# Kernel tuning notes

Measured on AMD Instinct MI355X. Metric: run time of the kernel, lower is better.

## Reference

```python
import jax, jax.numpy as jnp
import numpy as np

NUM_HEADS = 16
HEAD_DIM = 128
NUM_KV_HEADS = 8
NUM_KV_GROUPS = 2
HIDDEN = 2048
SCALE = 0.5  # hardcoded in the original SDPA call


def _fixed_sincos_pos(E, H):
    # matches ReusedProjReconstructor._fixed_sincos_pos (H even here)
    half = H // 2
    freq = jnp.exp(-jnp.log(jnp.float32(10000.0)) * jnp.arange(half, dtype=jnp.float32) / half)
    pos = jnp.arange(E, dtype=jnp.float32)[:, None]
    ang = pos * freq[None, :]
    return jnp.concatenate([jnp.sin(ang), jnp.cos(ang)], axis=1)  # [E, H]


def setup_inputs() -> dict:
    key = jax.random.key(0)
    ks = jax.random.split(key, 8)
    B, M, H = 4, 2048, HIDDEN
    kv_dim = NUM_KV_HEADS * HEAD_DIM
    s = 0.02
    return {
        "mem_act": jax.random.normal(ks[0], (B, M, H), jnp.float32),
        "Wq": jax.random.normal(ks[1], (H, H), jnp.float32) * s,
        "bq": jax.random.normal(ks[2], (H,), jnp.float32) * s,
        "Wk": jax.random.normal(ks[3], (kv_dim, H), jnp.float32) * s,
        "bk": jax.random.normal(ks[4], (kv_dim,), jnp.float32) * s,
        "Wv": jax.random.normal(ks[5], (kv_dim, H), jnp.float32) * s,
        "bv": jax.random.normal(ks[6], (kv_dim,), jnp.float32) * s,
        "Wo": jax.random.normal(ks[7], (H, H), jnp.float32) * s,
        "E": 2048,
    }


def reference(mem_act, Wq, bq, Wk, bk, Wv, bv, Wo, E):
    B, M, H = mem_act.shape
    # positional query hidden, shared across batch (q_ln is Identity)
    q_hidden = _fixed_sincos_pos(E, H).astype(mem_act.dtype)  # [E, H]
    q = (q_hidden @ Wq.T + bq).reshape(E, NUM_HEADS, HEAD_DIM)          # [E, nh, hd]
    k = (mem_act @ Wk.T + bk).reshape(B, M, NUM_KV_HEADS, HEAD_DIM)     # [B, M, nkv, hd]
    v = (mem_act @ Wv.T + bv).reshape(B, M, NUM_KV_HEADS, HEAD_DIM)
    # GQA: repeat kv heads (repeat_interleave over head dim)
    k = jnp.repeat(k, NUM_KV_GROUPS, axis=2)  # [B, M, nh, hd]
    v = jnp.repeat(v, NUM_KV_GROUPS, axis=2)
    # non-causal SDPA with scale=0.5, query broadcast over batch
    scores = jnp.einsum("ehd,bmhd->bhem", q, k) * SCALE  # [B, nh, E, M]
    attn = jax.nn.softmax(scores, axis=-1)
    out = jnp.einsum("bhem,bmhd->behd", attn, v).reshape(B, E, H)
    pred = out @ Wo.T  # o_proj (no bias, Qwen2 style)
    return pred
```

## Files before the change

### kernel.cpp

```cpp
#include <hip/hip_runtime.h>
#include <hip/hip_bf16.h>

typedef __attribute__((ext_vector_type(8))) short short8;
typedef __attribute__((ext_vector_type(4))) float f32x4;
typedef __attribute__((ext_vector_type(16))) float f32x16;
typedef unsigned short ushort_t;

__device__ __forceinline__ unsigned short f2bf(float x) {
    unsigned int u = __builtin_bit_cast(unsigned int, x);
    unsigned int r = (u + 0x7fffu + ((u >> 16) & 1u)) >> 16;
    return (unsigned short)r;
}

__device__ __forceinline__ void gload_lds16(const ushort_t* g, ushort_t* l) {
    __builtin_amdgcn_global_load_lds(
        (const __attribute__((address_space(1))) void*)g,
        (__attribute__((address_space(3))) void*)l, 16, 0, 0);
}

#define MFMA16(A, B, C) __builtin_amdgcn_mfma_f32_16x16x32_bf16((A), (B), (C), 0, 0, 0)
#define MFMA32(A, B, C) __builtin_amdgcn_mfma_f32_32x32x16_bf16((A), (B), (C), 0, 0, 0)

__global__ __launch_bounds__(256) void prep_all(const float* __restrict__ im,
                                                const float* __restrict__ iq,
                                                const float* __restrict__ ik,
                                                const float* __restrict__ iv,
                                                const float* __restrict__ io,
                                                ushort_t* __restrict__ om,
                                                ushort_t* __restrict__ oq,
                                                ushort_t* __restrict__ ok,
                                                ushort_t* __restrict__ ov,
                                                ushort_t* __restrict__ oo,
                                                ushort_t* __restrict__ qh) {
    const int bid = blockIdx.x;
    if (bid < 14336) {
        long i = ((long)bid * 256 + threadIdx.x) << 3;
        const float* s;
        ushort_t* d;
        if (i < 16777216)      { s = im + i;              d = om + i; }
        else if (i < 20971520) { s = iq + (i - 16777216); d = oq + (i - 16777216); }
        else if (i < 23068672) { s = ik + (i - 20971520); d = ok + (i - 20971520); }
        else if (i < 25165824) { s = iv + (i - 23068672); d = ov + (i - 23068672); }
        else                   { s = io + (i - 25165824); d = oo + (i - 25165824); }
        const float4* p = (const float4*)s;
        float4 a = p[0], b = p[1];
        short8 o;
        o[0] = (short)f2bf(a.x); o[1] = (short)f2bf(a.y);
        o[2] = (short)f2bf(a.z); o[3] = (short)f2bf(a.w);
        o[4] = (short)f2bf(b.x); o[5] = (short)f2bf(b.y);
        o[6] = (short)f2bf(b.z); o[7] = (short)f2bf(b.w);
        *(short8*)d = o;
    } else {
        const int t8 = (bid - 14336) * 256 + threadIdx.x;
        const int e = t8 >> 7;
        const int i0 = (t8 & 127) << 3;
        short8 sv8, cv8;
#pragma unroll
        for (int j = 0; j < 8; ++j) {
            const int i = i0 + j;
            float freq = __expf(-9.2103403719761836f * (float)i * (1.0f / 1024.0f));
            float ang = (float)e * freq;
            float rev = ang * 0.15915494309189535f;
            rev -= floorf(rev);
            float sv, cv;
            asm("v_sin_f32 %0, %1" : "=v"(sv) : "v"(rev));
            asm("v_cos_f32 %0, %1" : "=v"(cv) : "v"(rev));
            sv8[j] = (short)f2bf(sv);
            cv8[j] = (short)f2bf(cv);
        }
        *(short8*)(qh + (size_t)e * 2048 + i0)        = sv8;
        *(short8*)(qh + (size_t)e * 2048 + 1024 + i0) = cv8;
    }
}

__global__ __launch_bounds__(256, 2) void gemm_q(const ushort_t* __restrict__ A,
                                                 const ushort_t* __restrict__ Bw,
                                                 const float* __restrict__ bias,
                                                 ushort_t* __restrict__ Cout,
                                                 int M, int N, int K) {
    __shared__ ushort_t As[4][128 * 32];
    __shared__ ushort_t Bs[4][128 * 32];
    const int tid = threadIdx.x, lane = tid & 63;
    const int wid = tid >> 6;
    const int q5 = lane & 31, hi = lane >> 5;
    const int wm = wid >> 1, wn = wid & 1;
    const int nbn = N >> 7;
    const int nwg = gridDim.x;
    const int swz = (blockIdx.x & 7) * (nwg >> 3) + (blockIdx.x >> 3);
    const int bm = swz / nbn, bn = swz % nbn;
    const int row0 = bm << 7, col0 = bn << 7;
    const int NT = K >> 5;

    f32x16 acc[2][2];
#pragma unroll
    for (int mi = 0; mi < 2; ++mi)
#pragma unroll
        for (int nj = 0; nj < 2; ++nj)
#pragma unroll
            for (int rr = 0; rr < 16; ++rr) acc[mi][nj][rr] = 0.f;

    auto STAGE_HALF = [&](int buf, int kt, int i) {
        const int k0 = kt << 5;
        const int fb = (i * 256 + tid) << 4;
        const int rp = fb >> 7;
        const int bo = ((fb >> 4) & 7) ^ (rp & 7);
        const int row = rp * 2 + (bo >> 2);
        const int kc = (bo & 3) << 3;
        gload_lds16(A  + (size_t)(row0 + row) * K + k0 + kc, &As[buf][0] + (fb >> 1));
        gload_lds16(Bw + (size_t)(col0 + row) * K + k0 + kc, &Bs[buf][0] + (fb >> 1));
    };

    STAGE_HALF(0, 0, 0); STAGE_HALF(0, 0, 1);
    STAGE_HALF(1, 1, 0); STAGE_HALF(1, 1, 1);
    STAGE_HALF(2, 2, 0); STAGE_HALF(2, 2, 1);
    asm volatile("s_waitcnt vmcnt(8)" ::: "memory");
    __builtin_amdgcn_sched_barrier(0);
    __builtin_amdgcn_s_barrier();
    __builtin_amdgcn_sched_barrier(0);

    for (int t = 0; t < NT; ++t) {
        const int buf = t & 3;
        const char* Ab = (const char*)&As[buf][0];
        const char* Bb = (const char*)&Bs[buf][0];
#pragma unroll
        for (int ph = 0; ph < 2; ++ph) {
            short8 af[2], bfr[2];
#pragma unroll
            for (int nj = 0; nj < 2; ++nj) {
                const int col = wn * 64 + nj * 32 + q5;
                const int rp = col >> 1;
                const int blk = (((col & 1) << 2) + ph * 2 + hi) ^ (rp & 7);
                bfr[nj] = *(const short8*)(Bb + rp * 128 + blk * 16);
            }
#pragma unroll
            for (int mi = 0; mi < 2; ++mi) {
                const int row = wm * 64 + mi * 32 + q5;
                const int rp = row >> 1;
                const int blk = (((row & 1) << 2) + ph * 2 + hi) ^ (rp & 7);
                af[mi] = *(const short8*)(Ab + rp * 128 + blk * 16);
            }
            if (t + 3 < NT) STAGE_HALF((t + 3) & 3, t + 3, ph);
            __builtin_amdgcn_s_setprio(1);
#pragma unroll
            for (int mi = 0; mi < 2; ++mi)
#pragma unroll
                for (int nj = 0; nj < 2; ++nj)
                    acc[mi][nj] = MFMA32(af[mi], bfr[nj], acc[mi][nj]);
            __builtin_amdgcn_s_setprio(0);
        }

        if (t + 3 < NT) {
            asm volatile("s_waitcnt vmcnt(8)" ::: "memory");
        } else if (t + 2 < NT) {
            asm volatile("s_waitcnt vmcnt(4)" ::: "memory");
        } else if (t + 1 < NT) {
            asm volatile("s_waitcnt vmcnt(0)" ::: "memory");
        }
        if (t + 1 < NT) {
            __builtin_amdgcn_sched_barrier(0);
            __builtin_amdgcn_s_barrier();
            __builtin_amdgcn_sched_barrier(0);
        }
    }

#pragma unroll
    for (int mi = 0; mi < 2; ++mi)
#pragma unroll
        for (int nj = 0; nj < 2; ++nj) {
            const int col = col0 + wn * 64 + nj * 32 + q5;
            const float bv = bias[col];
#pragma unroll
            for (int rr = 0; rr < 16; ++rr) {
                const int row = row0 + wm * 64 + mi * 32 + (rr & 3) + 8 * (rr >> 2) + 4 * hi;
                Cout[(size_t)row * N + col] = f2bf((acc[mi][nj][rr] + bv) * 0.5f);
            }
        }
}

template <int EPI>
__global__ __launch_bounds__(512, 1) void gemm256(const ushort_t* __restrict__ A,
                                                  const ushort_t* __restrict__ Bw,
                                                  const float* __restrict__ b0,
                                                  const float* __restrict__ b1,
                                                  void* __restrict__ C0,
                                                  void* __restrict__ C1,
                                                  int M, int N, int K) {
    __shared__ ushort_t As[2][256 * 64];
    __shared__ ushort_t Bs[2][256 * 64];
    const int tid = threadIdx.x, lane = tid & 63;
    const int wid = tid >> 6;
    const int q5 = lane & 31, hi = lane >> 5;
    const int wm = wid >> 2, wn = wid & 3;
    const int nbn = N >> 8;
    const int nwg = gridDim.x;
    const int swz = (blockIdx.x & 7) * (nwg >> 3) + (blockIdx.x >> 3);
    const int bm = swz / nbn, bn = swz % nbn;
    const int row0 = bm << 8, col0 = bn << 8;
    const int NT = K >> 6;

    f32x16 acc[4][2];
#pragma unroll
    for (int mi = 0; mi < 4; ++mi)
#pragma unroll
        for (int nj = 0; nj < 2; ++nj)
#pragma unroll
            for (int rr = 0; rr < 16; ++rr) acc[mi][nj][rr] = 0.f;

    auto STAGE = [&](int buf, int kt) {
        const int k0 = kt << 6;
#pragma unroll
        for (int i = 0; i < 4; ++i) {
            const int fb = (i * 512 + tid) << 4;
            const int row = fb >> 7;
            const int blk = (fb >> 4) & 7;
            const int kc = ((blk ^ (row & 7)) << 3);
            gload_lds16(A  + (size_t)(row0 + row) * K + k0 + kc, &As[buf][0] + (fb >> 1));
            gload_lds16(Bw + (size_t)(col0 + row) * K + k0 + kc, &Bs[buf][0] + (fb >> 1));
        }
    };

    STAGE(0, 0);
    asm volatile("s_waitcnt vmcnt(0)" ::: "memory");
    __builtin_amdgcn_sched_barrier(0);
    __builtin_amdgcn_s_barrier();
    __builtin_amdgcn_sched_barrier(0);

    for (int t = 0; t < NT; ++t) {
        const int buf = t & 1;
        const char* Ab = (const char*)&As[buf][0];
        const char* Bb = (const char*)&Bs[buf][0];
        if (t + 1 < NT) STAGE(buf ^ 1, t + 1);
#pragma unroll
        for (int kk = 0; kk < 4; ++kk) {
            short8 af[4], bfr[2];
#pragma unroll
            for (int nj = 0; nj < 2; ++nj) {
                const int col = wn * 64 + nj * 32 + q5;
                const int blk = (kk * 2 + hi) ^ (col & 7);
                bfr[nj] = *(const short8*)(Bb + col * 128 + blk * 16);
            }
#pragma unroll
            for (int mi = 0; mi < 4; ++mi) {
                const int row = wm * 128 + mi * 32 + q5;
                const int blk = (kk * 2 + hi) ^ (row & 7);
                af[mi] = *(const short8*)(Ab + row * 128 + blk * 16);
            }
            __builtin_amdgcn_s_setprio(1);
#pragma unroll
            for (int mi = 0; mi < 4; ++mi)
#pragma unroll
                for (int nj = 0; nj < 2; ++nj)
                    acc[mi][nj] = MFMA32(af[mi], bfr[nj], acc[mi][nj]);
            __builtin_amdgcn_s_setprio(0);
        }

        if (t + 1 < NT) {
            asm volatile("s_waitcnt vmcnt(0)" ::: "memory");
            __builtin_amdgcn_sched_barrier(0);
            __builtin_amdgcn_s_barrier();
            __builtin_amdgcn_sched_barrier(0);
        }
    }

#pragma unroll
    for (int mi = 0; mi < 4; ++mi)
#pragma unroll
        for (int nj = 0; nj < 2; ++nj) {
            const int col = col0 + wn * 64 + nj * 32 + q5;
            if (EPI == 2) {
                float* outp = (float*)C0;
#pragma unroll
                for (int rr = 0; rr < 16; ++rr) {
                    const int row = row0 + wm * 128 + mi * 32 + (rr & 3) + 8 * (rr >> 2) + 4 * hi;
                    outp[(size_t)row * N + col] = acc[mi][nj][rr];
                }
            } else {
                if (col < 1024) {
                    const float bv = b0[col];
                    ushort_t* Kp = (ushort_t*)C0;
#pragma unroll
                    for (int rr = 0; rr < 16; ++rr) {
                        const int row = row0 + wm * 128 + mi * 32 + (rr & 3) + 8 * (rr >> 2) + 4 * hi;
                        Kp[(size_t)row * 1024 + col] = f2bf(acc[mi][nj][rr] + bv);
                    }
                } else {
                    const int vcol = col - 1024;
                    const float bv = b1[vcol];
                    ushort_t* Vt = (ushort_t*)C1;
#pragma unroll
                    for (int G = 0; G < 4; ++G) {
                        const int m0 = row0 + wm * 128 + mi * 32 + G * 8 + 4 * hi;
                        const int bb = m0 >> 11;
                        const int mm = m0 & 2047;
                        const size_t vtrow = (size_t)(bb * 8 + (vcol >> 7)) * 128 + (vcol & 127);
                        unsigned int p0 = (unsigned int)f2bf(acc[mi][nj][G * 4 + 0] + bv)
                                        | ((unsigned int)f2bf(acc[mi][nj][G * 4 + 1] + bv) << 16);
                        unsigned int p1 = (unsigned int)f2bf(acc[mi][nj][G * 4 + 2] + bv)
                                        | ((unsigned int)f2bf(acc[mi][nj][G * 4 + 3] + bv) << 16);
                        uint2 pk; pk.x = p0; pk.y = p1;
                        *(uint2*)(Vt + vtrow * 2048 + mm) = pk;
                    }
                }
            }
        }
}

__global__ __launch_bounds__(512, 2) void attn_kernel(const ushort_t* __restrict__ Q,
                                                      const ushort_t* __restrict__ Kg,
                                                      const ushort_t* __restrict__ Vt,
                                                      ushort_t* __restrict__ O) {
    __shared__ ushort_t Ks[2][64 * 128];
    __shared__ ushort_t Vts[2][128 * 64];

    const int tid = threadIdx.x, lane = tid & 63, wid = tid >> 6;
    const int q5 = lane & 31;
    const int hi = lane >> 5;
    const int wq = wid & 3;
    const int wg = (blockIdx.x & 7) * 64 + (blockIdx.x >> 3);
    const int bkvh = wg >> 4;
    const int etile = wg & 15;
    const int b = bkvh >> 3, kvh = bkvh & 7;
    const int h = kvh * 2 + (wid >> 2);
    const int e0 = etile * 128;
    const int qrow = e0 + wq * 32 + q5;

    short8 Qf[8];
    {
        const ushort_t* qp = Q + (size_t)qrow * 2048 + h * 128 + hi * 8;
#pragma unroll
        for (int c = 0; c < 8; ++c) Qf[c] = *(const short8*)(qp + c * 16);
    }

    unsigned aK[2][8];
#pragma unroll
    for (int h2 = 0; h2 < 2; ++h2) {
        const int key = h2 * 32 + q5;
#pragma unroll
        for (int c = 0; c < 8; ++c)
            aK[h2][c] = key * 256 + (((c * 2 + hi) ^ (key & 7)) << 4);
    }
    unsigned aV[4];
#pragma unroll
    for (int c16 = 0; c16 < 4; ++c16)
        aV[c16] = q5 * 128 + (((c16 * 2 + hi) ^ (q5 & 7)) << 4);

    float lrow = 0.f;
    f32x16 oacc[4];
#pragma unroll
    for (int d0 = 0; d0 < 4; ++d0)
#pragma unroll
        for (int r = 0; r < 16; ++r) oacc[d0][r] = 0.f;

    f32x16 Z16;
#pragma unroll
    for (int r = 0; r < 16; ++r) Z16[r] = 0.f;

    const ushort_t* Kbase  = Kg + (size_t)b * 2048 * 1024 + kvh * 128;
    const ushort_t* Vtbase = Vt + (size_t)bkvh * 128 * 2048;

    auto STAGE = [&](int buf, int kv0) {
#pragma unroll
        for (int i = 0; i < 2; ++i) {
            const int fb = (i * 8 + wid) * 1024 + lane * 16;
            const int key = fb >> 8;
            const int blk = (fb >> 4) & 15;
            gload_lds16(Kbase + (size_t)(kv0 + key) * 1024 + ((blk ^ (key & 7)) << 3),
                        &Ks[buf][0] + (fb >> 1));
            const int d = fb >> 7;
            const int kb = (fb >> 4) & 7;
            gload_lds16(Vtbase + (size_t)d * 2048 + kv0 + ((kb ^ (d & 7)) << 3),
                        &Vts[buf][0] + (fb >> 1));
        }
    };

    auto TILE = [&](int bo) {
        f32x16 sS[2];
        __builtin_amdgcn_s_setprio(1);
#pragma unroll
        for (int c = 0; c < 8; ++c) {
            short8 ka0 = *(const short8*)((const char*)Ks + bo + aK[0][c]);
            short8 ka1 = *(const short8*)((const char*)Ks + bo + aK[1][c]);
            sS[0] = MFMA32(ka0, Qf[c], (c == 0) ? Z16 : sS[0]);
            sS[1] = MFMA32(ka1, Qf[c], (c == 0) ? Z16 : sS[1]);
        }
        __builtin_amdgcn_s_setprio(0);

#pragma unroll
        for (int h2 = 0; h2 < 2; ++h2)
#pragma unroll
            for (int r = 0; r < 16; ++r) sS[h2][r] = __expf(sS[h2][r]);

        float ts[16];
#pragma unroll
        for (int i = 0; i < 8; ++i) ts[i] = sS[0][2 * i] + sS[0][2 * i + 1];
#pragma unroll
        for (int i = 0; i < 8; ++i) ts[8 + i] = sS[1][2 * i] + sS[1][2 * i + 1];
#pragma unroll
        for (int s = 8; s > 0; s >>= 1)
#pragma unroll
            for (int i = 0; i < s; ++i) ts[i] += ts[i + s];
        lrow += ts[0] + __shfl_xor(ts[0], 32);

        unsigned int W[2][4][2];
#pragma unroll
        for (int h2 = 0; h2 < 2; ++h2)
#pragma unroll
            for (int q4 = 0; q4 < 4; ++q4)
#pragma unroll
                for (int p = 0; p < 2; ++p) {
                    unsigned int w;
                    asm("v_cvt_pk_bf16_f32 %0, %1, %2"
                        : "=v"(w)
                        : "v"(sS[h2][q4 * 4 + 2 * p]), "v"(sS[h2][q4 * 4 + 2 * p + 1]));
                    W[h2][q4][p] = w;
                }

#pragma unroll
        for (int c16 = 0; c16 < 4; ++c16) {
            const int h2 = c16 >> 1;
            const int q4a = (c16 & 1) * 2, q4b = q4a + 1;
            auto r0 = __builtin_amdgcn_permlane32_swap(W[h2][q4a][0], W[h2][q4b][0], false, false);
            auto r1 = __builtin_amdgcn_permlane32_swap(W[h2][q4a][1], W[h2][q4b][1], false, false);
            union { unsigned int w[4]; short8 v; } pa;
            pa.w[0] = r0[0];
            pa.w[1] = r1[0];
            pa.w[2] = r0[1];
            pa.w[3] = r1[1];
            __builtin_amdgcn_s_setprio(1);
#pragma unroll
            for (int d0 = 0; d0 < 4; ++d0) {
                short8 vb = *(const short8*)((const char*)Vts + bo + aV[c16] + d0 * 4096);
                oacc[d0] = MFMA32(pa.v, vb, oacc[d0]);
            }
            __builtin_amdgcn_s_setprio(0);
        }
    };

    STAGE(0, 0);
    __syncthreads();

#pragma unroll 1
    for (int tt = 0; tt < 16; ++tt) {
        STAGE(1, (2 * tt + 1) * 64);
        TILE(0);
        __syncthreads();
        if (tt < 15) STAGE(0, (2 * tt + 2) * 64);
        TILE(16384);
        __syncthreads();
    }

#pragma unroll
    for (int reg = 0; reg < 16; ++reg) {
        const int qr = (reg & 3) + 8 * (reg >> 2) + 4 * hi;
        const float lr = __shfl(lrow, qr);
        const float inv = 1.0f / lr;
        const int e = e0 + wq * 32 + qr;
        ushort_t* op = O + ((size_t)b * 2048 + e) * 2048 + h * 128 + q5;
#pragma unroll
        for (int d0 = 0; d0 < 4; ++d0)
            op[d0 * 32] = f2bf(oacc[d0][reg] * inv);
    }
}

extern "C" void kernel_launch(void* const* d_in, const int* in_sizes, int n_in,
                              void* d_out, int out_size, void* d_ws, size_t ws_size,
                              hipStream_t stream) {
    const float* mem_act = (const float*)d_in[0];
    const float* Wq = (const float*)d_in[1];
    const float* bq = (const float*)d_in[2];
    const float* Wk = (const float*)d_in[3];
    const float* bk = (const float*)d_in[4];
    const float* Wv = (const float*)d_in[5];
    const float* bv = (const float*)d_in[6];
    const float* Wo = (const float*)d_in[7];
    float* out = (float*)d_out;

    char* w = (char*)d_ws;
    ushort_t* memb = (ushort_t*)w; w += (size_t)16777216 * 2;
    ushort_t* wqb  = (ushort_t*)w; w += (size_t)4194304 * 2;
    ushort_t* wkvb = (ushort_t*)w; w += (size_t)4194304 * 2;
    ushort_t* wob  = (ushort_t*)w; w += (size_t)4194304 * 2;
    ushort_t* qh   = (ushort_t*)w; w += (size_t)4194304 * 2;
    ushort_t* Qp   = (ushort_t*)w; w += (size_t)4194304 * 2;
    ushort_t* Kp   = (ushort_t*)w; w += (size_t)8388608 * 2;
    ushort_t* Vtp  = (ushort_t*)w; w += (size_t)8388608 * 2;
    ushort_t* AO   = (ushort_t*)w; w += (size_t)16777216 * 2;

    dim3 blk(256);
    prep_all<<<15360, blk, 0, stream>>>(mem_act, Wq, Wk, Wv, Wo,
                                        memb, wqb, wkvb, wkvb + (size_t)2097152, wob, qh);

    gemm_q<<<16 * 16, blk, 0, stream>>>(qh, wqb, bq, Qp, 2048, 2048, 2048);

    gemm256<0><<<256, dim3(512), 0, stream>>>(memb, wkvb, bk, bv, Kp, Vtp, 8192, 2048, 2048);

    attn_kernel<<<512, dim3(512), 0, stream>>>(Qp, Kp, Vtp, AO);

    gemm256<2><<<256, dim3(512), 0, stream>>>(AO, wob, nullptr, nullptr, out, nullptr, 8192, 2048, 2048);
}
```

Before: 357.8 us.

## Fuse Q projection GEMM into KV projection kernel launch

Merges the separate Q projection GEMM into the KV projection kernel by assigning the extra 256 blocks to compute Q with a 128x128 tile and 512 threads. This removes one kernel launch and lets the Q work fill the device alongside the KV GEMM. Because each block reserves the full LDS and only one block fits per CU, the Q blocks may simply run as a second wave rather than overlapping.

```diff
diff --git a/kernel.cpp b/kernel.cpp
--- a/kernel.cpp
+++ b/kernel.cpp
@@ -18,7 +18,6 @@
         (__attribute__((address_space(3))) void*)l, 16, 0, 0);
 }
 
-#define MFMA16(A, B, C) __builtin_amdgcn_mfma_f32_16x16x32_bf16((A), (B), (C), 0, 0, 0)
 #define MFMA32(A, B, C) __builtin_amdgcn_mfma_f32_32x32x16_bf16((A), (B), (C), 0, 0, 0)
 
 __global__ __launch_bounds__(256) void prep_all(const float* __restrict__ im,
@@ -73,208 +72,100 @@
     }
 }
 
-__global__ __launch_bounds__(256, 2) void gemm_q(const ushort_t* __restrict__ A,
-                                                 const ushort_t* __restrict__ Bw,
-                                                 const float* __restrict__ bias,
-                                                 ushort_t* __restrict__ Cout,
-                                                 int M, int N, int K) {
-    __shared__ ushort_t As[4][128 * 32];
-    __shared__ ushort_t Bs[4][128 * 32];
-    const int tid = threadIdx.x, lane = tid & 63;
-    const int wid = tid >> 6;
-    const int q5 = lane & 31, hi = lane >> 5;
-    const int wm = wid >> 1, wn = wid & 1;
-    const int nbn = N >> 7;
-    const int nwg = gridDim.x;
-    const int swz = (blockIdx.x & 7) * (nwg >> 3) + (blockIdx.x >> 3);
-    const int bm = swz / nbn, bn = swz % nbn;
-    const int row0 = bm << 7, col0 = bn << 7;
-    const int NT = K >> 5;
-
-    f32x16 acc[2][2];
-#pragma unroll
-    for (int mi = 0; mi < 2; ++mi)
-#pragma unroll
-        for (int nj = 0; nj < 2; ++nj)
-#pragma unroll
-            for (int rr = 0; rr < 16; ++rr) acc[mi][nj][rr] = 0.f;
-
-    auto STAGE_HALF = [&](int buf, int kt, int i) {
-        const int k0 = kt << 5;
-        const int fb = (i * 256 + tid) << 4;
-        const int rp = fb >> 7;
-        const int bo = ((fb >> 4) & 7) ^ (rp & 7);
-        const int row = rp * 2 + (bo >> 2);
-        const int kc = (bo & 3) << 3;
-        gload_lds16(A  + (size_t)(row0 + row) * K + k0 + kc, &As[buf][0] + (fb >> 1));
-        gload_lds16(Bw + (size_t)(col0 + row) * K + k0 + kc, &Bs[buf][0] + (fb >> 1));
-    };
-
-    STAGE_HALF(0, 0, 0); STAGE_HALF(0, 0, 1);
-    STAGE_HALF(1, 1, 0); STAGE_HALF(1, 1, 1);
-    STAGE_HALF(2, 2, 0); STAGE_HALF(2, 2, 1);
-    asm volatile("s_waitcnt vmcnt(8)" ::: "memory");
-    __builtin_amdgcn_sched_barrier(0);
-    __builtin_amdgcn_s_barrier();
-    __builtin_amdgcn_sched_barrier(0);
-
-    for (int t = 0; t < NT; ++t) {
-        const int buf = t & 3;
-        const char* Ab = (const char*)&As[buf][0];
-        const char* Bb = (const char*)&Bs[buf][0];
-#pragma unroll
-        for (int ph = 0; ph < 2; ++ph) {
-            short8 af[2], bfr[2];
-#pragma unroll
-            for (int nj = 0; nj < 2; ++nj) {
-                const int col = wn * 64 + nj * 32 + q5;
-                const int rp = col >> 1;
-                const int blk = (((col & 1) << 2) + ph * 2 + hi) ^ (rp & 7);
-                bfr[nj] = *(const short8*)(Bb + rp * 128 + blk * 16);
-            }
-#pragma unroll
-            for (int mi = 0; mi < 2; ++mi) {
-                const int row = wm * 64 + mi * 32 + q5;
-                const int rp = row >> 1;
-                const int blk = (((row & 1) << 2) + ph * 2 + hi) ^ (rp & 7);
-                af[mi] = *(const short8*)(Ab + rp * 128 + blk * 16);
-            }
-            if (t + 3 < NT) STAGE_HALF((t + 3) & 3, t + 3, ph);
-            __builtin_amdgcn_s_setprio(1);
-#pragma unroll
-            for (int mi = 0; mi < 2; ++mi)
-#pragma unroll
-                for (int nj = 0; nj < 2; ++nj)
-                    acc[mi][nj] = MFMA32(af[mi], bfr[nj], acc[mi][nj]);
-            __builtin_amdgcn_s_setprio(0);
-        }
-
-        if (t + 3 < NT) {
-            asm volatile("s_waitcnt vmcnt(8)" ::: "memory");
-        } else if (t + 2 < NT) {
-            asm volatile("s_waitcnt vmcnt(4)" ::: "memory");
-        } else if (t + 1 < NT) {
-            asm volatile("s_waitcnt vmcnt(0)" ::: "memory");
-        }
-        if (t + 1 < NT) {
-            __builtin_amdgcn_sched_barrier(0);
-            __builtin_amdgcn_s_barrier();
-            __builtin_amdgcn_sched_barrier(0);
-        }
-    }
-
-#pragma unroll
-    for (int mi = 0; mi < 2; ++mi)
-#pragma unroll
-        for (int nj = 0; nj < 2; ++nj) {
-            const int col = col0 + wn * 64 + nj * 32 + q5;
-            const float bv = bias[col];
-#pragma unroll
-            for (int rr = 0; rr < 16; ++rr) {
-                const int row = row0 + wm * 64 + mi * 32 + (rr & 3) + 8 * (rr >> 2) + 4 * hi;
-                Cout[(size_t)row * N + col] = f2bf((acc[mi][nj][rr] + bv) * 0.5f);
-            }
-        }
-}
-
-template <int EPI>
-__global__ __launch_bounds__(512, 1) void gemm256(const ushort_t* __restrict__ A,
-                                                  const ushort_t* __restrict__ Bw,
-                                                  const float* __restrict__ b0,
-                                                  const float* __restrict__ b1,
-                                                  void* __restrict__ C0,
-                                                  void* __restrict__ C1,
-                                                  int M, int N, int K) {
+__global__ __launch_bounds__(512, 1) void kvq_fused(const ushort_t* __restrict__ A,
+                                                    const ushort_t* __restrict__ Bw,
+                                                    const float* __restrict__ b0,
+                                                    const float* __restrict__ b1,
+                                                    void* __restrict__ C0,
+                                                    void* __restrict__ C1,
+                                                    const ushort_t* __restrict__ Qh,
+                                                    const ushort_t* __restrict__ Wq,
+                                                    const float* __restrict__ bq,
+                                                    ushort_t* __restrict__ Qp) {
     __shared__ ushort_t As[2][256 * 64];
     __shared__ ushort_t Bs[2][256 * 64];
     const int tid = threadIdx.x, lane = tid & 63;
     const int wid = tid >> 6;
     const int q5 = lane & 31, hi = lane >> 5;
-    const int wm = wid >> 2, wn = wid & 3;
-    const int nbn = N >> 8;
-    const int nwg = gridDim.x;
-    const int swz = (blockIdx.x & 7) * (nwg >> 3) + (blockIdx.x >> 3);
-    const int bm = swz / nbn, bn = swz % nbn;
-    const int row0 = bm << 8, col0 = bn << 8;
-    const int NT = K >> 6;
-
-    f32x16 acc[4][2];
-#pragma unroll
-    for (int mi = 0; mi < 4; ++mi)
-#pragma unroll
-        for (int nj = 0; nj < 2; ++nj)
-#pragma unroll
-            for (int rr = 0; rr < 16; ++rr) acc[mi][nj][rr] = 0.f;
-
-    auto STAGE = [&](int buf, int kt) {
-        const int k0 = kt << 6;
-#pragma unroll
-        for (int i = 0; i < 4; ++i) {
-            const int fb = (i * 512 + tid) << 4;
-            const int row = fb >> 7;
-            const int blk = (fb >> 4) & 7;
-            const int kc = ((blk ^ (row & 7)) << 3);
-            gload_lds16(A  + (size_t)(row0 + row) * K + k0 + kc, &As[buf][0] + (fb >> 1));
-            gload_lds16(Bw + (size_t)(col0 + row) * K + k0 + kc, &Bs[buf][0] + (fb >> 1));
-        }
-    };
-
-    STAGE(0, 0);
-    asm volatile("s_waitcnt vmcnt(0)" ::: "memory");
-    __builtin_amdgcn_sched_barrier(0);
-    __builtin_amdgcn_s_barrier();
-    __builtin_amdgcn_sched_barrier(0);
-
-    for (int t = 0; t < NT; ++t) {
-        const int buf = t & 1;
-        const char* Ab = (const char*)&As[buf][0];
-        const char* Bb = (const char*)&Bs[buf][0];
-        if (t + 1 < NT) STAGE(buf ^ 1, t + 1);
-#pragma unroll
-        for (int kk = 0; kk < 4; ++kk) {
-            short8 af[4], bfr[2];
+
+    if (blockIdx.x < 256) {
+        const int M = 8192, N = 2048, K = 2048;
+        const int wm = wid >> 2, wn = wid & 3;
+        const int nbn = N >> 8;
+        const int swz = (blockIdx.x & 7) * 32 + (blockIdx.x >> 3);
+        const int bm = swz / nbn, bn = swz % nbn;
+        const int row0 = bm << 8, col0 = bn << 8;
+        const int NT = K >> 6;
+
+        f32x16 acc[4][2];
+#pragma unroll
+        for (int mi = 0; mi < 4; ++mi)
+#pragma unroll
+            for (int nj = 0; nj < 2; ++nj)
+#pragma unroll
+                for (int rr = 0; rr < 16; ++rr) acc[mi][nj][rr] = 0.f;
+
+        auto STAGE = [&](int buf, int kt) {
+            const int k0 = kt << 6;
+#pragma unroll
+            for (int i = 0; i < 4; ++i) {
+                const int fb = (i * 512 + tid) << 4;
+                const int row = fb >> 7;
+                const int blk = (fb >> 4) & 7;
+                const int kc = ((blk ^ (row & 7)) << 3);
+                gload_lds16(A  + (size_t)(row0 + row) * K + k0 + kc, &As[buf][0] + (fb >> 1));
+                gload_lds16(Bw + (size_t)(col0 + row) * K + k0 + kc, &Bs[buf][0] + (fb >> 1));
+            }
+        };
+
+        STAGE(0, 0);
+        asm volatile("s_waitcnt vmcnt(0)" ::: "memory");
+        __builtin_amdgcn_sched_barrier(0);
+        __builtin_amdgcn_s_barrier();
+        __builtin_amdgcn_sched_barrier(0);
+
+        for (int t = 0; t < NT; ++t) {
+            const int buf = t & 1;
+            const char* Ab = (const char*)&As[buf][0];
+            const char* Bb = (const char*)&Bs[buf][0];
+            if (t + 1 < NT) STAGE(buf ^ 1, t + 1);
+#pragma unroll
+            for (int kk = 0; kk < 4; ++kk) {
+                short8 af[4], bfr[2];
+#pragma unroll
+                for (int nj = 0; nj < 2; ++nj) {
+                    const int col = wn * 64 + nj * 32 + q5;
+                    const int blk = (kk * 2 + hi) ^ (col & 7);
+                    bfr[nj] = *(const short8*)(Bb + col * 128 + blk * 16);
+                }
+#pragma unroll
+                for (int mi = 0; mi < 4; ++mi) {
+                    const int row = wm * 128 + mi * 32 + q5;
+                    const int blk = (kk * 2 + hi) ^ (row & 7);
+                    af[mi] = *(const short8*)(Ab + row * 128 + blk * 16);
+                }
+                __builtin_amdgcn_s_setprio(1);
+#pragma unroll
+                for (int mi = 0; mi < 4; ++mi)
+#pragma unroll
+                    for (int nj = 0; nj < 2; ++nj)
+                        acc[mi][nj] = MFMA32(af[mi], bfr[nj], acc[mi][nj]);
+                __builtin_amdgcn_s_setprio(0);
+            }
+
+            if (t + 1 < NT) {
+                asm volatile("s_waitcnt vmcnt(0)" ::: "memory");
+                __builtin_amdgcn_sched_barrier(0);
+                __builtin_amdgcn_s_barrier();
+                __builtin_amdgcn_sched_barrier(0);
+            }
+        }
+
+#pragma unroll
+        for (int mi = 0; mi < 4; ++mi)
 #pragma unroll
             for (int nj = 0; nj < 2; ++nj) {
-                const int col = wn * 64 + nj * 32 + q5;
-                const int blk = (kk * 2 + hi) ^ (col & 7);
-                bfr[nj] = *(const short8*)(Bb + col * 128 + blk * 16);
-            }
-#pragma unroll
-            for (int mi = 0; mi < 4; ++mi) {
-                const int row = wm * 128 + mi * 32 + q5;
-                const int blk = (kk * 2 + hi) ^ (row & 7);
-                af[mi] = *(const short8*)(Ab + row * 128 + blk * 16);
-            }
-            __builtin_amdgcn_s_setprio(1);
-#pragma unroll
-            for (int mi = 0; mi < 4; ++mi)
-#pragma unroll
-                for (int nj = 0; nj < 2; ++nj)
-                    acc[mi][nj] = MFMA32(af[mi], bfr[nj], acc[mi][nj]);
-            __builtin_amdgcn_s_setprio(0);
-        }
-
-        if (t + 1 < NT) {
-            asm volatile("s_waitcnt vmcnt(0)" ::: "memory");
-            __builtin_amdgcn_sched_barrier(0);
-            __builtin_amdgcn_s_barrier();
-            __builtin_amdgcn_sched_barrier(0);
-        }
-    }
-
-#pragma unroll
-    for (int mi = 0; mi < 4; ++mi)
-#pragma unroll
-        for (int nj = 0; nj < 2; ++nj) {
-            const int col = col0 + wn * 64 + nj * 32 + q5;
-            if (EPI == 2) {
-                float* outp = (float*)C0;
-#pragma unroll
-                for (int rr = 0; rr < 16; ++rr) {
-                    const int row = row0 + wm * 128 + mi * 32 + (rr & 3) + 8 * (rr >> 2) + 4 * hi;
-                    outp[(size_t)row * N + col] = acc[mi][nj][rr];
-                }
-            } else {
+                const int col = col0 + wn * 64 + nj * 32 + q5;
                 if (col < 1024) {
                     const float bv = b0[col];
                     ushort_t* Kp = (ushort_t*)C0;
@@ -302,6 +193,187 @@
                     }
                 }
             }
+    } else {
+        const int N = 2048, K = 2048;
+        const int wm = wid >> 2, wn = wid & 3;
+        const int qb = blockIdx.x - 256;
+        const int swz = (qb & 7) * 32 + (qb >> 3);
+        const int bm = swz >> 4, bn = swz & 15;
+        const int row0 = bm << 7, col0 = bn << 7;
+        const int NT = K >> 5;
+
+        ushort_t* Aqb = &As[0][0];
+        ushort_t* Bqb = &As[1][0];
+
+        f32x16 acc[2];
+#pragma unroll
+        for (int mi = 0; mi < 2; ++mi)
+#pragma unroll
+            for (int rr = 0; rr < 16; ++rr) acc[mi][rr] = 0.f;
+
+        auto STAGE_Q = [&](int buf, int kt) {
+            const int k0 = kt << 5;
+            const int fb = tid << 4;
+            const int rp = fb >> 7;
+            const int bo = ((fb >> 4) & 7) ^ (rp & 7);
+            const int row = rp * 2 + (bo >> 2);
+            const int kc = (bo & 3) << 3;
+            gload_lds16(Qh + (size_t)(row0 + row) * K + k0 + kc, Aqb + buf * 4096 + (fb >> 1));
+            gload_lds16(Wq + (size_t)(col0 + row) * K + k0 + kc, Bqb + buf * 4096 + (fb >> 1));
+        };
+
+        STAGE_Q(0, 0); STAGE_Q(1, 1); STAGE_Q(2, 2);
+        asm volatile("s_waitcnt vmcnt(4)" ::: "memory");
+        __builtin_amdgcn_sched_barrier(0);
+        __builtin_amdgcn_s_barrier();
+        __builtin_amdgcn_sched_barrier(0);
+
+        for (int t = 0; t < NT; ++t) {
+            const int buf = t & 3;
+            const char* Ab = (const char*)(Aqb + buf * 4096);
+            const char* Bb = (const char*)(Bqb + buf * 4096);
+#pragma unroll
+            for (int ph = 0; ph < 2; ++ph) {
+                short8 af[2], bfr;
+                {
+                    const int col = wn * 32 + q5;
+                    const int rp = col >> 1;
+                    const int blk = (((col & 1) << 2) + ph * 2 + hi) ^ (rp & 7);
+                    bfr = *(const short8*)(Bb + rp * 128 + blk * 16);
+                }
+#pragma unroll
+                for (int mi = 0; mi < 2; ++mi) {
+                    const int row = wm * 64 + mi * 32 + q5;
+                    const int rp = row >> 1;
+                    const int blk = (((row & 1) << 2) + ph * 2 + hi) ^ (rp & 7);
+                    af[mi] = *(const short8*)(Ab + rp * 128 + blk * 16);
+                }
+                if (ph == 0 && t + 3 < NT) STAGE_Q((t + 3) & 3, t + 3);
+                __builtin_amdgcn_s_setprio(1);
+#pragma unroll
+                for (int mi = 0; mi < 2; ++mi)
+                    acc[mi] = MFMA32(af[mi], bfr, acc[mi]);
+                __builtin_amdgcn_s_setprio(0);
+            }
+
+            if (t + 3 < NT) {
+                asm volatile("s_waitcnt vmcnt(4)" ::: "memory");
+            } else if (t + 2 < NT) {
+                asm volatile("s_waitcnt vmcnt(2)" ::: "memory");
+            } else if (t + 1 < NT) {
+                asm volatile("s_waitcnt vmcnt(0)" ::: "memory");
+            }
+            if (t + 1 < NT) {
+                __builtin_amdgcn_sched_barrier(0);
+                __builtin_amdgcn_s_barrier();
+                __builtin_amdgcn_sched_barrier(0);
+            }
+        }
+
+#pragma unroll
+        for (int mi = 0; mi < 2; ++mi) {
+            const int col = col0 + wn * 32 + q5;
+            const float bv = bq[col];
+#pragma unroll
+            for (int rr = 0; rr < 16; ++rr) {
+                const int row = row0 + wm * 64 + mi * 32 + (rr & 3) + 8 * (rr >> 2) + 4 * hi;
+                Qp[(size_t)row * N + col] = f2bf((acc[mi][rr] + bv) * 0.5f);
+            }
+        }
+    }
+}
+
+__global__ __launch_bounds__(512, 1) void gemm256o(const ushort_t* __restrict__ A,
+                                                   const ushort_t* __restrict__ Bw,
+                                                   float* __restrict__ C0,
+                                                   int M, int N, int K) {
+    __shared__ ushort_t As[2][256 * 64];
+    __shared__ ushort_t Bs[2][256 * 64];
+    const int tid = threadIdx.x, lane = tid & 63;
+    const int wid = tid >> 6;
+    const int q5 = lane & 31, hi = lane >> 5;
+    const int wm = wid >> 2, wn = wid & 3;
+    const int nbn = N >> 8;
+    const int nwg = gridDim.x;
+    const int swz = (blockIdx.x & 7) * (nwg >> 3) + (blockIdx.x >> 3);
+    const int bm = swz / nbn, bn = swz % nbn;
+    const int row0 = bm << 8, col0 = bn << 8;
+    const int NT = K >> 6;
+
+    f32x16 acc[4][2];
+#pragma unroll
+    for (int mi = 0; mi < 4; ++mi)
+#pragma unroll
+        for (int nj = 0; nj < 2; ++nj)
+#pragma unroll
+            for (int rr = 0; rr < 16; ++rr) acc[mi][nj][rr] = 0.f;
+
+    auto STAGE = [&](int buf, int kt) {
+        const int k0 = kt << 6;
+#pragma unroll
+        for (int i = 0; i < 4; ++i) {
+            const int fb = (i * 512 + tid) << 4;
+            const int row = fb >> 7;
+            const int blk = (fb >> 4) & 7;
+            const int kc = ((blk ^ (row & 7)) << 3);
+            gload_lds16(A  + (size_t)(row0 + row) * K + k0 + kc, &As[buf][0] + (fb >> 1));
+            gload_lds16(Bw + (size_t)(col0 + row) * K + k0 + kc, &Bs[buf][0] + (fb >> 1));
+        }
+    };
+
+    STAGE(0, 0);
+    asm volatile("s_waitcnt vmcnt(0)" ::: "memory");
+    __builtin_amdgcn_sched_barrier(0);
+    __builtin_amdgcn_s_barrier();
+    __builtin_amdgcn_sched_barrier(0);
+
+    for (int t = 0; t < NT; ++t) {
+        const int buf = t & 1;
+        const char* Ab = (const char*)&As[buf][0];
+        const char* Bb = (const char*)&Bs[buf][0];
+        if (t + 1 < NT) STAGE(buf ^ 1, t + 1);
+#pragma unroll
+        for (int kk = 0; kk < 4; ++kk) {
+            short8 af[4], bfr[2];
+#pragma unroll
+            for (int nj = 0; nj < 2; ++nj) {
+                const int col = wn * 64 + nj * 32 + q5;
+                const int blk = (kk * 2 + hi) ^ (col & 7);
+                bfr[nj] = *(const short8*)(Bb + col * 128 + blk * 16);
+            }
+#pragma unroll
+            for (int mi = 0; mi < 4; ++mi) {
+                const int row = wm * 128 + mi * 32 + q5;
+                const int blk = (kk * 2 + hi) ^ (row & 7);
+                af[mi] = *(const short8*)(Ab + row * 128 + blk * 16);
+            }
+            __builtin_amdgcn_s_setprio(1);
+#pragma unroll
+            for (int mi = 0; mi < 4; ++mi)
+#pragma unroll
+                for (int nj = 0; nj < 2; ++nj)
+                    acc[mi][nj] = MFMA32(af[mi], bfr[nj], acc[mi][nj]);
+            __builtin_amdgcn_s_setprio(0);
+        }
+
+        if (t + 1 < NT) {
+            asm volatile("s_waitcnt vmcnt(0)" ::: "memory");
+            __builtin_amdgcn_sched_barrier(0);
+            __builtin_amdgcn_s_barrier();
+            __builtin_amdgcn_sched_barrier(0);
+        }
+    }
+
+#pragma unroll
+    for (int mi = 0; mi < 4; ++mi)
+#pragma unroll
+        for (int nj = 0; nj < 2; ++nj) {
+            const int col = col0 + wn * 64 + nj * 32 + q5;
+#pragma unroll
+            for (int rr = 0; rr < 16; ++rr) {
+                const int row = row0 + wm * 128 + mi * 32 + (rr & 3) + 8 * (rr >> 2) + 4 * hi;
+                C0[(size_t)row * N + col] = acc[mi][nj][rr];
+            }
         }
 }
 
@@ -490,11 +562,10 @@
     prep_all<<<15360, blk, 0, stream>>>(mem_act, Wq, Wk, Wv, Wo,
                                         memb, wqb, wkvb, wkvb + (size_t)2097152, wob, qh);
 
-    gemm_q<<<16 * 16, blk, 0, stream>>>(qh, wqb, bq, Qp, 2048, 2048, 2048);
-
-    gemm256<0><<<256, dim3(512), 0, stream>>>(memb, wkvb, bk, bv, Kp, Vtp, 8192, 2048, 2048);
+    kvq_fused<<<512, dim3(512), 0, stream>>>(memb, wkvb, bk, bv, Kp, Vtp,
+                                             qh, wqb, bq, Qp);
 
     attn_kernel<<<512, dim3(512), 0, stream>>>(Qp, Kp, Vtp, AO);
 
-    gemm256<2><<<256, dim3(512), 0, stream>>>(AO, wob, nullptr, nullptr, out, nullptr, 8192, 2048, 2048);
-}
+    gemm256o<<<256, dim3(512), 0, stream>>>(AO, wob, out, 8192, 2048, 2048);
+}
```

After: 360.9 us. About the same (+0.8%).
